# Kernel tuning notes

Measured on AMD Instinct MI355X. Metric: run time of the kernel, lower is better.

Reference implementation:

```python
import jax, jax.numpy as jnp
import numpy as np

L = 0.24        # diffusion step size (diffuse() default)
K = 0.03        # exp(logk) with logk = log(0.03) for feature_extractor='none'
EPS = 1e-8
NSTEPS = 128    # number of diffusion iterations (Npre)
SCALE = 4       # H/sh super-resolution factor (512/128)


def _g(x, k=K):
    return 1.0 / (1.0 + jnp.abs(x * x) / (k * k))


def _c(I, k=K):
    # I: [B, C, H, W] guide features; channel-mean abs finite differences -> edge-stopping coeffs
    cv = _g(jnp.mean(jnp.abs(I[:, :, 1:, :] - I[:, :, :-1, :]), axis=1, keepdims=True), k)  # [B,1,H-1,W]
    ch = _g(jnp.mean(jnp.abs(I[:, :, :, 1:] - I[:, :, :, :-1]), axis=1, keepdims=True), k)  # [B,1,H,W-1]
    return cv, ch


def _diffuse_step(cv, ch, I, l=L):
    # dv/dh computed from the ORIGINAL I (matches torch: both diffs taken before in-place updates,
    # and the in-place +/- updates commute since tv/th are fixed).
    dv = I[:, :, 1:, :] - I[:, :, :-1, :]
    dh = I[:, :, :, 1:] - I[:, :, :, :-1]
    tv = l * cv * dv
    th = l * ch * dh
    I = I.at[:, :, 1:, :].add(-tv).at[:, :, :-1, :].add(tv)
    I = I.at[:, :, :, 1:].add(-th).at[:, :, :, :-1].add(th)
    return I


def _adjust_step(img, source, mask_inv, eps=EPS):
    B, C, H, W = img.shape
    sh, sw = H // SCALE, W // SCALE
    # AdaptiveAvgPool2d((sh, sw)) with exact integer factor == block mean
    img_ss = img.reshape(B, C, sh, SCALE, sw, SCALE).mean(axis=(3, 5))
    ratio_ss = source / (img_ss + eps)
    ratio_ss = jnp.where(mask_inv, jnp.ones_like(ratio_ss), ratio_ss)
    # F.interpolate(mode='nearest') with exact integer factor == repeat
    ratio = jnp.repeat(jnp.repeat(ratio_ss, SCALE, axis=2), SCALE, axis=3)
    return img * ratio


def _diffuse(img, guide, source, mask_inv):
    guide_feats = jnp.concatenate([img, guide], axis=1)  # feature_extractor='none' path
    cv, ch = _c(guide_feats, K)

    def step(I, _):
        I = _diffuse_step(cv, ch, I, L)
        I = _adjust_step(I, source, mask_inv, EPS)
        return I, None

    img, _ = jax.lax.scan(step, img, None, length=NSTEPS)
    return img, cv, ch


def setup_inputs() -> dict:
    key = jax.random.key(0)
    k1, k2, k3, k4 = jax.random.split(key, 4)
    guide = jax.random.normal(k1, (2, 3, 512, 512), dtype=jnp.float32)
    # depth values kept positive and > deps=0.1 so the shift branch in forward() is not taken
    y_bicubic = jax.random.uniform(k2, (2, 1, 512, 512), dtype=jnp.float32) + 0.5
    source = jax.random.uniform(k3, (2, 1, 128, 128), dtype=jnp.float32) + 0.5
    mask_lr = jax.random.uniform(k4, (2, 1, 128, 128), dtype=jnp.float32)
    return {"guide": guide, "y_bicubic": y_bicubic, "source": source, "mask_lr": mask_lr}


def reference(guide, y_bicubic, source, mask_lr):
    mask_inv = mask_lr > 0.5
    y_pred, cv, ch = _diffuse(y_bicubic, guide, source, mask_inv)
    return y_pred, cv, ch
```

## Files before the change

kernel.cpp:

```cpp
#include <hip/hip_runtime.h>

constexpr int Hh = 512, Ww = 512, Bn = 2;
constexpr int SWs = 128;
constexpr float Lf = 0.24f;
constexpr float Kf = 0.03f;
constexpr float EPSf = 1e-8f;
constexpr int NSTEPS = 128;

constexpr int NPIX = Bn * Hh * Ww;
constexpr int CVN  = Bn * (Hh - 1) * Ww;

constexpr int OT = 32;
constexpr int KS = 5;
constexpr int HALO = 4 * KS;
constexpr int G = (OT + 2 * HALO) / 4;
constexpr int NREC = G * G;
constexpr int REC = 20;
constexpr int BUFSZ = NREC * REC;
constexpr int NWG = Bn * (Hh / OT) * (Ww / OT);
constexpr int CREC = 40;

__device__ __forceinline__ int clampi(int v, int lo, int hi) {
  return min(max(v, lo), hi);
}
__device__ __forceinline__ int recof(int t) { return t * REC; }

__global__ __launch_bounds__(256) void cvch_kernel(
    const float* __restrict__ img, const float* __restrict__ guide,
    float* __restrict__ cv, float* __restrict__ ch) {
  int idx = blockIdx.x * blockDim.x + threadIdx.x;
  if (idx >= NPIX) return;
  int x = idx & (Ww - 1);
  int y = (idx >> 9) & (Hh - 1);
  int b = idx >> 18;
  const float inv_k2 = 1.0f / (Kf * Kf);
  const float* f0 = img + (size_t)b * Hh * Ww;
  const float* g0 = guide + (size_t)b * 3 * Hh * Ww;
  const float* g1 = g0 + Hh * Ww;
  const float* g2 = g1 + Hh * Ww;
  int p = y * Ww + x;
  float c0 = f0[p], c1 = g0[p], c2 = g1[p], c3 = g2[p];
  if (y < Hh - 1) {
    int q = p + Ww;
    float m = (fabsf(f0[q] - c0) + fabsf(g0[q] - c1) +
               fabsf(g1[q] - c2) + fabsf(g2[q] - c3)) * 0.25f;
    cv[(b * (Hh - 1) + y) * Ww + x] = 1.0f / (1.0f + m * m * inv_k2);
  }
  if (x < Ww - 1) {
    int q = p + 1;
    float m = (fabsf(f0[q] - c0) + fabsf(g0[q] - c1) +
               fabsf(g1[q] - c2) + fabsf(g2[q] - c3)) * 0.25f;
    ch[(b * Hh + y) * (Ww - 1) + x] = 1.0f / (1.0f + m * m * inv_k2);
  }
}

__global__ __launch_bounds__(256) void coefpack_kernel(
    const float* __restrict__ cv, const float* __restrict__ ch,
    float* __restrict__ crec) {
  int wg = blockIdx.x;
  int b  = wg >> 8;
  int t  = wg & 255;
  int Ty0 = (t >> 4) * OT;
  int Tx0 = (t & 15) * OT;
  int tid = threadIdx.x;
  int by = 1 + (tid >> 4), bx = 1 + (tid & 15);
  int gy0 = Ty0 - HALO + 4 * by;
  int gx0 = Tx0 - HALO + 4 * bx;

  const float* cvb = cv + (size_t)b * (Hh - 1) * Ww;
  const float* chb = ch + (size_t)b * Hh * (Ww - 1);
  float* r = crec + ((size_t)wg * 256 + tid) * CREC;

#pragma unroll
  for (int k = 0; k < 5; ++k) {
    int ro = gy0 - 1 + k;
    float4 o;
    if (ro < 0 || ro > Hh - 2) {
      o = make_float4(0.f, 0.f, 0.f, 0.f);
    } else if (gx0 < 0) {
      float v = Lf * cvb[ro * Ww];
      o = make_float4(v, v, v, v);
    } else if (gx0 > Ww - 4) {
      float v = Lf * cvb[ro * Ww + Ww - 1];
      o = make_float4(v, v, v, v);
    } else {
      float4 t4 = *reinterpret_cast<const float4*>(&cvb[ro * Ww + gx0]);
      o = make_float4(Lf * t4.x, Lf * t4.y, Lf * t4.z, Lf * t4.w);
    }
    *reinterpret_cast<float4*>(r + 4 * k) = o;
  }
#pragma unroll
  for (int rr = 0; rr < 4; ++rr) {
    int ri = clampi(gy0 + rr, 0, Hh - 1);
#pragma unroll
    for (int j = 0; j < 5; ++j) {
      int e = gx0 - 1 + j;
      r[20 + rr * 5 + j] =
          (e >= 0 && e <= Ww - 2) ? Lf * chb[ri * (Ww - 1) + e] : 0.0f;
    }
  }
}

__global__ __launch_bounds__(256, 3) void diffuse5_kernel(
    const float* __restrict__ src, float* __restrict__ dst,
    const float* __restrict__ crec,
    const float* __restrict__ source, const float* __restrict__ mask,
    int nsteps) {
  __shared__ __align__(16) float ebuf[2 * BUFSZ];

  int wg = blockIdx.x;
  int b  = wg >> 8;
  int t  = wg & 255;
  int Ty0 = (t >> 4) * OT;
  int Tx0 = (t & 15) * OT;

  int tid = threadIdx.x;
  int by = 1 + (tid >> 4), bx = 1 + (tid & 15);
  int gy0 = Ty0 - HALO + 4 * by;
  int gx0 = Tx0 - HALO + 4 * bx;

  int blk = by * G + bx;
  int oMy = recof(blk);
  int oU  = recof(blk - G) + 4;
  int oD  = recof(blk + G) + 0;
  int oL  = recof(blk - 1) + 12;
  int oR  = recof(blk + 1) + 8;

  const size_t ib = (size_t)b * Hh * Ww;
  const float* S = src + ib;
  float* D = dst + ib;

  auto ld4 = [&](int gy, int gx) -> float4 {
    gy = clampi(gy, 0, Hh - 1);
    if (gx < 0)      { float v = S[gy * Ww];          return make_float4(v, v, v, v); }
    if (gx > Ww - 4) { float v = S[gy * Ww + Ww - 1]; return make_float4(v, v, v, v); }
    return *reinterpret_cast<const float4*>(&S[gy * Ww + gx]);
  };

  float cvk[5][4];
  float chk[4][5];
  {
    const float* r = crec + ((size_t)wg * 256 + tid) * CREC;
#pragma unroll
    for (int k = 0; k < 5; ++k) {
      float4 t4 = *reinterpret_cast<const float4*>(r + 4 * k);
      cvk[k][0] = t4.x; cvk[k][1] = t4.y; cvk[k][2] = t4.z; cvk[k][3] = t4.w;
    }
#pragma unroll
    for (int q = 0; q < 5; ++q) {
      float4 t4 = *reinterpret_cast<const float4*>(r + 20 + 4 * q);
      chk[0][0 + 0] = (q == 0) ? t4.x : chk[0][0];
    }
#pragma unroll
    for (int rr = 0; rr < 4; ++rr)
#pragma unroll
      for (int j = 0; j < 5; ++j) chk[rr][j] = r[20 + rr * 5 + j];
  }

  float I[4][4];
#pragma unroll
  for (int r = 0; r < 4; ++r) {
    float4 t4 = ld4(gy0 + r, gx0);
    I[r][0] = t4.x; I[r][1] = t4.y; I[r][2] = t4.z; I[r][3] = t4.w;
  }
  float nT[4], nB[4], nL[4], nR[4];
  {
    float4 t4 = ld4(gy0 - 1, gx0);
    nT[0] = t4.x; nT[1] = t4.y; nT[2] = t4.z; nT[3] = t4.w;
    t4 = ld4(gy0 + 4, gx0);
    nB[0] = t4.x; nB[1] = t4.y; nB[2] = t4.z; nB[3] = t4.w;
    int cL = clampi(gx0 - 1, 0, Ww - 1), cR = clampi(gx0 + 4, 0, Ww - 1);
#pragma unroll
    for (int r = 0; r < 4; ++r) {
      int gy = clampi(gy0 + r, 0, Hh - 1);
      nL[r] = S[gy * Ww + cL];
      nR[r] = S[gy * Ww + cR];
    }
  }

  int sy = clampi(gy0 >> 2, 0, SWs - 1);
  int sx = clampi(gx0 >> 2, 0, SWs - 1);
  int sidx = (b * SWs + sy) * SWs + sx;
  float srcv = source[sidx];
  bool mskv = mask[sidx] > 0.5f;

#pragma unroll
  for (int s = 0; s < KS; ++s) {
    if (s >= nsteps) break;
    if (s > 0) {
      const float* eb = ebuf + ((s - 1) & 1) * BUFSZ;
      float4 t4;
      t4 = *reinterpret_cast<const float4*>(eb + oU);
      nT[0] = t4.x; nT[1] = t4.y; nT[2] = t4.z; nT[3] = t4.w;
      t4 = *reinterpret_cast<const float4*>(eb + oD);
      nB[0] = t4.x; nB[1] = t4.y; nB[2] = t4.z; nB[3] = t4.w;
      t4 = *reinterpret_cast<const float4*>(eb + oL);
      nL[0] = t4.x; nL[1] = t4.y; nL[2] = t4.z; nL[3] = t4.w;
      t4 = *reinterpret_cast<const float4*>(eb + oR);
      nR[0] = t4.x; nR[1] = t4.y; nR[2] = t4.z; nR[3] = t4.w;
    }

    float V[4][4];
    float sum = 0.0f;
#pragma unroll
    for (int r = 0; r < 4; ++r)
#pragma unroll
      for (int c = 0; c < 4; ++c) {
        float cc = I[r][c];
        float up = (r == 0) ? nT[c] : I[r - 1][c];
        float dn = (r == 3) ? nB[c] : I[r + 1][c];
        float lf = (c == 0) ? nL[r] : I[r][c - 1];
        float rt = (c == 3) ? nR[r] : I[r][c + 1];
        float acc = cc + cvk[r + 1][c] * (dn - cc) - cvk[r][c] * (cc - up)
                       + chk[r][c + 1] * (rt - cc) - chk[r][c] * (cc - lf);
        V[r][c] = acc;
        sum += acc;
      }
    float ratio = mskv ? 1.0f : __fdividef(srcv, sum * 0.0625f + EPSf);
#pragma unroll
    for (int r = 0; r < 4; ++r)
#pragma unroll
      for (int c = 0; c < 4; ++c) I[r][c] = V[r][c] * ratio;

    if (s == nsteps - 1) {
      if (by >= 5 && by < 13 && bx >= 5 && bx < 13) {
#pragma unroll
        for (int r = 0; r < 4; ++r)
          *reinterpret_cast<float4*>(&D[(gy0 + r) * Ww + gx0]) =
              make_float4(I[r][0], I[r][1], I[r][2], I[r][3]);
      }
    } else {
      float* eb = ebuf + (s & 1) * BUFSZ;
      if (by > s && by < G - 1 - s && bx > s && bx < G - 1 - s) {
        *reinterpret_cast<float4*>(eb + oMy + 0) =
            make_float4(I[0][0], I[0][1], I[0][2], I[0][3]);
        *reinterpret_cast<float4*>(eb + oMy + 4) =
            make_float4(I[3][0], I[3][1], I[3][2], I[3][3]);
        *reinterpret_cast<float4*>(eb + oMy + 8) =
            make_float4(I[0][0], I[1][0], I[2][0], I[3][0]);
        *reinterpret_cast<float4*>(eb + oMy + 12) =
            make_float4(I[0][3], I[1][3], I[2][3], I[3][3]);
      }
      __syncthreads();
    }
  }
}

constexpr int FT = 32;
__global__ __launch_bounds__(64) void step_kernel(
    const float* __restrict__ src, float* __restrict__ dst,
    const float* __restrict__ cv, const float* __restrict__ ch,
    const float* __restrict__ source, const float* __restrict__ mask) {
  __shared__ float sIl[FT + 2][FT + 3];
  int b = blockIdx.z;
  int ty0 = blockIdx.y * FT, tx0 = blockIdx.x * FT;
  const float* I = src + (size_t)b * Hh * Ww;
  int tid = threadIdx.x;
  for (int i = tid; i < (FT + 2) * (FT + 2); i += 64) {
    int ly = i / (FT + 2), lx = i % (FT + 2);
    int gy = max(0, min(Hh - 1, ty0 + ly - 1));
    int gx = max(0, min(Ww - 1, tx0 + lx - 1));
    sIl[ly][lx] = I[gy * Ww + gx];
  }
  __syncthreads();
  int bby = tid >> 3, bbx = tid & 7;
  int py0 = bby * 4, px0 = bbx * 4;
  int gy0 = ty0 + py0, gx0 = tx0 + px0;
  const float* cvb = cv + (size_t)b * (Hh - 1) * Ww;
  const float* chb = ch + (size_t)b * Hh * (Ww - 1);
  float v[4][4]; float sum = 0.0f;
#pragma unroll
  for (int dy = 0; dy < 4; ++dy) {
    int y = gy0 + dy, ly = py0 + dy + 1;
#pragma unroll
    for (int dx = 0; dx < 4; ++dx) {
      int x = gx0 + dx, lx = px0 + dx + 1;
      float cc = sIl[ly][lx];
      float acc = cc;
      if (y < Hh - 1) acc += Lf * cvb[y * Ww + x] * (sIl[ly + 1][lx] - cc);
      if (y > 0)      acc -= Lf * cvb[(y - 1) * Ww + x] * (cc - sIl[ly - 1][lx]);
      if (x < Ww - 1) acc += Lf * chb[y * (Ww - 1) + x] * (sIl[ly][lx + 1] - cc);
      if (x > 0)      acc -= Lf * chb[y * (Ww - 1) + x - 1] * (cc - sIl[ly][lx - 1]);
      v[dy][dx] = acc; sum += acc;
    }
  }
  int sidx = (b * SWs + (gy0 >> 2)) * SWs + (gx0 >> 2);
  float ratio = (mask[sidx] > 0.5f) ? 1.0f : source[sidx] / (sum * 0.0625f + EPSf);
  float* D = dst + (size_t)b * Hh * Ww;
#pragma unroll
  for (int dy = 0; dy < 4; ++dy)
    *reinterpret_cast<float4*>(&D[(gy0 + dy) * Ww + gx0]) =
        make_float4(v[dy][0] * ratio, v[dy][1] * ratio,
                    v[dy][2] * ratio, v[dy][3] * ratio);
}

extern "C" void kernel_launch(void* const* d_in, const int* in_sizes, int n_in,
                              void* d_out, int out_size, void* d_ws, size_t ws_size,
                              hipStream_t stream) {
  const float* guide  = (const float*)d_in[0];
  const float* ybic   = (const float*)d_in[1];
  const float* source = (const float*)d_in[2];
  const float* mask   = (const float*)d_in[3];

  float* out   = (float*)d_out;
  float* ypred = out;
  float* cv    = out + NPIX;
  float* ch    = out + NPIX + CVN;

  cvch_kernel<<<dim3((NPIX + 255) / 256), dim3(256), 0, stream>>>(ybic, guide, cv, ch);

  size_t needPing = (size_t)2 * NPIX * sizeof(float);
  size_t needCoef = (size_t)NWG * 256 * CREC * sizeof(float);

  if (ws_size >= needPing + needCoef) {
    float* wsb0 = (float*)d_ws;
    float* wsb1 = wsb0 + NPIX;
    float* crec = wsb1 + NPIX;
    coefpack_kernel<<<dim3(NWG), dim3(256), 0, stream>>>(cv, ch, crec);
    const float* sp = ybic;
    int done = 0, l = 0;
    while (done < NSTEPS) {
      int ns = (NSTEPS - done >= KS) ? KS : (NSTEPS - done);
      bool lastL = (done + ns == NSTEPS);
      float* dp = lastL ? ypred : ((l & 1) ? wsb1 : wsb0);
      diffuse5_kernel<<<dim3(NWG), dim3(256), 0, stream>>>(sp, dp, crec,
                                                           source, mask, ns);
      sp = dp; done += ns; ++l;
    }
  } else {
    float* wsbuf = (float*)d_ws;
    dim3 grid(Ww / FT, Hh / FT, Bn);
    const float* sp = ybic;
    for (int it = 0; it < NSTEPS; ++it) {
      float* dp = (it & 1) ? ypred : wsbuf;
      step_kernel<<<grid, dim3(64), 0, stream>>>(sp, dp, cv, ch, source, mask);
      sp = dp;
    }
  }
}
```

Before: 306.3 us.

## Fuse eight diffusion steps per launch with a larger halo and single LDS buffer

Raises the temporal blocking depth from five to eight steps per launch, so the halo grows to 32 pixels and the workgroup grows to 512 threads (484 active 4x4 blocks). The double-buffered shared edge buffer becomes a single buffer with an extra barrier before each write. The initial edges are staged through shared memory, with global loads only at the outer ring. The number of launches drops from 26 to 16 and global traffic per step falls, at the cost of more redundant halo compute (the tile area ratio goes from 2.25 to 4) and larger coefficient records.

```diff
diff --git a/kernel.cpp b/kernel.cpp
--- a/kernel.cpp
+++ b/kernel.cpp
@@ -11,13 +11,15 @@
 constexpr int CVN  = Bn * (Hh - 1) * Ww;
 
 constexpr int OT = 32;
-constexpr int KS = 5;
+constexpr int KS = 8;
 constexpr int HALO = 4 * KS;
 constexpr int G = (OT + 2 * HALO) / 4;
-constexpr int NREC = G * G;
+constexpr int GI = G - 2;
+constexpr int NB = GI * GI;
+constexpr int NTHR = 512;
 constexpr int REC = 20;
-constexpr int BUFSZ = NREC * REC;
 constexpr int NWG = Bn * (Hh / OT) * (Ww / OT);
+constexpr int NLAUNCH = NSTEPS / KS;
 constexpr int CREC = 40;
 
 __device__ __forceinline__ int clampi(int v, int lo, int hi) {
@@ -54,7 +56,7 @@
   }
 }
 
-__global__ __launch_bounds__(256) void coefpack_kernel(
+__global__ __launch_bounds__(NTHR) void coefpack_kernel(
     const float* __restrict__ cv, const float* __restrict__ ch,
     float* __restrict__ crec) {
   int wg = blockIdx.x;
@@ -63,13 +65,15 @@
   int Ty0 = (t >> 4) * OT;
   int Tx0 = (t & 15) * OT;
   int tid = threadIdx.x;
-  int by = 1 + (tid >> 4), bx = 1 + (tid & 15);
+  if (tid >= NB) return;
+  int iy = tid / GI, ix = tid - iy * GI;
+  int by = 1 + iy, bx = 1 + ix;
   int gy0 = Ty0 - HALO + 4 * by;
   int gx0 = Tx0 - HALO + 4 * bx;
 
   const float* cvb = cv + (size_t)b * (Hh - 1) * Ww;
   const float* chb = ch + (size_t)b * Hh * (Ww - 1);
-  float* r = crec + ((size_t)wg * 256 + tid) * CREC;
+  float* r = crec + ((size_t)wg * NTHR + tid) * CREC;
 
 #pragma unroll
   for (int k = 0; k < 5; ++k) {
@@ -101,12 +105,11 @@
   }
 }
 
-__global__ __launch_bounds__(256, 3) void diffuse5_kernel(
+__global__ __launch_bounds__(NTHR, 4) void diffuse8_kernel(
     const float* __restrict__ src, float* __restrict__ dst,
     const float* __restrict__ crec,
-    const float* __restrict__ source, const float* __restrict__ mask,
-    int nsteps) {
-  __shared__ __align__(16) float ebuf[2 * BUFSZ];
+    const float* __restrict__ source, const float* __restrict__ mask) {
+  __shared__ __align__(16) float ebuf[G * G * REC];
 
   int wg = blockIdx.x;
   int b  = wg >> 8;
@@ -115,7 +118,10 @@
   int Tx0 = (t & 15) * OT;
 
   int tid = threadIdx.x;
-  int by = 1 + (tid >> 4), bx = 1 + (tid & 15);
+  bool act = tid < NB;
+  int tt = min(tid, NB - 1);
+  int iy = tt / GI, ix = tt - iy * GI;
+  int by = 1 + iy, bx = 1 + ix;
   int gy0 = Ty0 - HALO + 4 * by;
   int gx0 = Tx0 - HALO + 4 * bx;
 
@@ -140,18 +146,13 @@
   float cvk[5][4];
   float chk[4][5];
   {
-    const float* r = crec + ((size_t)wg * 256 + tid) * CREC;
+    const float* r = crec + ((size_t)wg * NTHR + tid) * CREC;
 #pragma unroll
     for (int k = 0; k < 5; ++k) {
       float4 t4 = *reinterpret_cast<const float4*>(r + 4 * k);
       cvk[k][0] = t4.x; cvk[k][1] = t4.y; cvk[k][2] = t4.z; cvk[k][3] = t4.w;
     }
 #pragma unroll
-    for (int q = 0; q < 5; ++q) {
-      float4 t4 = *reinterpret_cast<const float4*>(r + 20 + 4 * q);
-      chk[0][0 + 0] = (q == 0) ? t4.x : chk[0][0];
-    }
-#pragma unroll
     for (int rr = 0; rr < 4; ++rr)
 #pragma unroll
       for (int j = 0; j < 5; ++j) chk[rr][j] = r[20 + rr * 5 + j];
@@ -162,20 +163,6 @@
   for (int r = 0; r < 4; ++r) {
     float4 t4 = ld4(gy0 + r, gx0);
     I[r][0] = t4.x; I[r][1] = t4.y; I[r][2] = t4.z; I[r][3] = t4.w;
-  }
-  float nT[4], nB[4], nL[4], nR[4];
-  {
-    float4 t4 = ld4(gy0 - 1, gx0);
-    nT[0] = t4.x; nT[1] = t4.y; nT[2] = t4.z; nT[3] = t4.w;
-    t4 = ld4(gy0 + 4, gx0);
-    nB[0] = t4.x; nB[1] = t4.y; nB[2] = t4.z; nB[3] = t4.w;
-    int cL = clampi(gx0 - 1, 0, Ww - 1), cR = clampi(gx0 + 4, 0, Ww - 1);
-#pragma unroll
-    for (int r = 0; r < 4; ++r) {
-      int gy = clampi(gy0 + r, 0, Hh - 1);
-      nL[r] = S[gy * Ww + cL];
-      nR[r] = S[gy * Ww + cR];
-    }
   }
 
   int sy = clampi(gy0 >> 2, 0, SWs - 1);
@@ -184,61 +171,93 @@
   float srcv = source[sidx];
   bool mskv = mask[sidx] > 0.5f;
 
+  if (act) {
+    *reinterpret_cast<float4*>(ebuf + oMy + 0) =
+        make_float4(I[0][0], I[0][1], I[0][2], I[0][3]);
+    *reinterpret_cast<float4*>(ebuf + oMy + 4) =
+        make_float4(I[3][0], I[3][1], I[3][2], I[3][3]);
+    *reinterpret_cast<float4*>(ebuf + oMy + 8) =
+        make_float4(I[0][0], I[1][0], I[2][0], I[3][0]);
+    *reinterpret_cast<float4*>(ebuf + oMy + 12) =
+        make_float4(I[0][3], I[1][3], I[2][3], I[3][3]);
+  }
+  __syncthreads();
+
+  float nT[4], nB[4], nL[4], nR[4];
+
 #pragma unroll
   for (int s = 0; s < KS; ++s) {
-    if (s >= nsteps) break;
-    if (s > 0) {
-      const float* eb = ebuf + ((s - 1) & 1) * BUFSZ;
+    {
       float4 t4;
-      t4 = *reinterpret_cast<const float4*>(eb + oU);
+      if (s == 0 && by == 1) t4 = ld4(gy0 - 1, gx0);
+      else t4 = *reinterpret_cast<const float4*>(ebuf + oU);
       nT[0] = t4.x; nT[1] = t4.y; nT[2] = t4.z; nT[3] = t4.w;
-      t4 = *reinterpret_cast<const float4*>(eb + oD);
+      if (s == 0 && by == GI) t4 = ld4(gy0 + 4, gx0);
+      else t4 = *reinterpret_cast<const float4*>(ebuf + oD);
       nB[0] = t4.x; nB[1] = t4.y; nB[2] = t4.z; nB[3] = t4.w;
-      t4 = *reinterpret_cast<const float4*>(eb + oL);
-      nL[0] = t4.x; nL[1] = t4.y; nL[2] = t4.z; nL[3] = t4.w;
-      t4 = *reinterpret_cast<const float4*>(eb + oR);
-      nR[0] = t4.x; nR[1] = t4.y; nR[2] = t4.z; nR[3] = t4.w;
-    }
-
-    float V[4][4];
+      if (s == 0 && bx == 1) {
+        int cL = clampi(gx0 - 1, 0, Ww - 1);
+#pragma unroll
+        for (int r = 0; r < 4; ++r)
+          nL[r] = S[clampi(gy0 + r, 0, Hh - 1) * Ww + cL];
+      } else {
+        t4 = *reinterpret_cast<const float4*>(ebuf + oL);
+        nL[0] = t4.x; nL[1] = t4.y; nL[2] = t4.z; nL[3] = t4.w;
+      }
+      if (s == 0 && bx == GI) {
+        int cR = clampi(gx0 + 4, 0, Ww - 1);
+#pragma unroll
+        for (int r = 0; r < 4; ++r)
+          nR[r] = S[clampi(gy0 + r, 0, Hh - 1) * Ww + cR];
+      } else {
+        t4 = *reinterpret_cast<const float4*>(ebuf + oR);
+        nR[0] = t4.x; nR[1] = t4.y; nR[2] = t4.z; nR[3] = t4.w;
+      }
+    }
+
     float sum = 0.0f;
-#pragma unroll
-    for (int r = 0; r < 4; ++r)
+    float rowOrig[4];
+#pragma unroll
+    for (int r = 0; r < 4; ++r) {
+      float leftOrig = 0.0f;
 #pragma unroll
       for (int c = 0; c < 4; ++c) {
         float cc = I[r][c];
-        float up = (r == 0) ? nT[c] : I[r - 1][c];
+        float up = (r == 0) ? nT[c] : rowOrig[c];
         float dn = (r == 3) ? nB[c] : I[r + 1][c];
-        float lf = (c == 0) ? nL[r] : I[r][c - 1];
+        float lf = (c == 0) ? nL[r] : leftOrig;
         float rt = (c == 3) ? nR[r] : I[r][c + 1];
         float acc = cc + cvk[r + 1][c] * (dn - cc) - cvk[r][c] * (cc - up)
                        + chk[r][c + 1] * (rt - cc) - chk[r][c] * (cc - lf);
-        V[r][c] = acc;
+        rowOrig[c] = cc;
+        leftOrig = cc;
+        I[r][c] = acc;
         sum += acc;
       }
+    }
     float ratio = mskv ? 1.0f : __fdividef(srcv, sum * 0.0625f + EPSf);
 #pragma unroll
     for (int r = 0; r < 4; ++r)
 #pragma unroll
-      for (int c = 0; c < 4; ++c) I[r][c] = V[r][c] * ratio;
-
-    if (s == nsteps - 1) {
-      if (by >= 5 && by < 13 && bx >= 5 && bx < 13) {
+      for (int c = 0; c < 4; ++c) I[r][c] *= ratio;
+
+    if (s == KS - 1) {
+      if (by >= KS && by < G - KS && bx >= KS && bx < G - KS) {
 #pragma unroll
         for (int r = 0; r < 4; ++r)
           *reinterpret_cast<float4*>(&D[(gy0 + r) * Ww + gx0]) =
               make_float4(I[r][0], I[r][1], I[r][2], I[r][3]);
       }
     } else {
-      float* eb = ebuf + (s & 1) * BUFSZ;
-      if (by > s && by < G - 1 - s && bx > s && bx < G - 1 - s) {
-        *reinterpret_cast<float4*>(eb + oMy + 0) =
+      __syncthreads();
+      if (act && by > s && by < G - 1 - s && bx > s && bx < G - 1 - s) {
+        *reinterpret_cast<float4*>(ebuf + oMy + 0) =
             make_float4(I[0][0], I[0][1], I[0][2], I[0][3]);
-        *reinterpret_cast<float4*>(eb + oMy + 4) =
+        *reinterpret_cast<float4*>(ebuf + oMy + 4) =
             make_float4(I[3][0], I[3][1], I[3][2], I[3][3]);
-        *reinterpret_cast<float4*>(eb + oMy + 8) =
+        *reinterpret_cast<float4*>(ebuf + oMy + 8) =
             make_float4(I[0][0], I[1][0], I[2][0], I[3][0]);
-        *reinterpret_cast<float4*>(eb + oMy + 12) =
+        *reinterpret_cast<float4*>(ebuf + oMy + 12) =
             make_float4(I[0][3], I[1][3], I[2][3], I[3][3]);
       }
       __syncthreads();
@@ -310,22 +329,19 @@
   cvch_kernel<<<dim3((NPIX + 255) / 256), dim3(256), 0, stream>>>(ybic, guide, cv, ch);
 
   size_t needPing = (size_t)2 * NPIX * sizeof(float);
-  size_t needCoef = (size_t)NWG * 256 * CREC * sizeof(float);
+  size_t needCoef = (size_t)NWG * NTHR * CREC * sizeof(float);
 
   if (ws_size >= needPing + needCoef) {
     float* wsb0 = (float*)d_ws;
     float* wsb1 = wsb0 + NPIX;
     float* crec = wsb1 + NPIX;
-    coefpack_kernel<<<dim3(NWG), dim3(256), 0, stream>>>(cv, ch, crec);
+    coefpack_kernel<<<dim3(NWG), dim3(NTHR), 0, stream>>>(cv, ch, crec);
     const float* sp = ybic;
-    int done = 0, l = 0;
-    while (done < NSTEPS) {
-      int ns = (NSTEPS - done >= KS) ? KS : (NSTEPS - done);
-      bool lastL = (done + ns == NSTEPS);
-      float* dp = lastL ? ypred : ((l & 1) ? wsb1 : wsb0);
-      diffuse5_kernel<<<dim3(NWG), dim3(256), 0, stream>>>(sp, dp, crec,
-                                                           source, mask, ns);
-      sp = dp; done += ns; ++l;
+    for (int l = 0; l < NLAUNCH; ++l) {
+      float* dp = (l == NLAUNCH - 1) ? ypred : ((l & 1) ? wsb1 : wsb0);
+      diffuse8_kernel<<<dim3(NWG), dim3(NTHR), 0, stream>>>(sp, dp, crec,
+                                                            source, mask);
+      sp = dp;
     }
   } else {
     float* wsbuf = (float*)d_ws;
```

Measured after the change: 567.8 us. 1.85x slower.
